# Kernel tuning notes

Hardware: AMD Instinct MI355X
Metric: run time of the kernel (lower is better)

The kernel has to match this reference:

```python
import jax, jax.numpy as jnp
import numpy as np

EPS = 1e-6

def elu_feature_map(x):
    return jax.nn.elu(x) + 1.0

def setup_inputs() -> dict:
    key = jax.random.key(0)
    kq, kk, kv = jax.random.split(key, 3)
    N, L, S, H, D = 8, 8192, 8192, 8, 32
    return {
        "queries": jax.random.normal(kq, (N, L, H, D), dtype=jnp.float32),
        "keys": jax.random.normal(kk, (N, S, H, D), dtype=jnp.float32),
        "values": jax.random.normal(kv, (N, S, H, D), dtype=jnp.float32),
    }

def reference(queries, keys, values):
    # Linear (kernelized) attention, default path of MixAttention.forward
    Q = elu_feature_map(queries)            # [N,L,H,D]
    K = elu_feature_map(keys)               # [N,S,H,D]
    v_length = values.shape[1]
    vals = values / v_length                # [N,S,H,D]
    KV = jnp.einsum('nshd,nshv->nhdv', K, vals)          # [N,H,D,D]
    Z = 1.0 / (jnp.einsum('nlhd,nhd->nlh', Q, K.sum(axis=1)) + EPS)  # [N,L,H]
    out = jnp.einsum('nlhd,nhdv,nlh->nlhv', Q, KV, Z) * v_length     # [N,L,H,D]
    return out
```

## Files before the change

kernel.cpp:

```cpp
#include <hip/hip_runtime.h>


constexpr int N_ = 8, L_ = 8192, S_ = 8192, H_ = 8, D_ = 32;
constexpr int NH = N_ * H_;
constexpr int PART_STRIDE = D_ * D_ + D_;
constexpr int LCH = 256;
constexpr float EPS_ = 1e-6f;
constexpr int HD = H_ * D_;
constexpr int CHUNK = 32;

__device__ __forceinline__ float fmap(float x) {
    return x > 0.0f ? x + 1.0f : __expf(x);
}

__device__ __forceinline__ void dma16(const float* g, float* l) {
    __builtin_amdgcn_global_load_lds(
        (const __attribute__((address_space(1))) unsigned int*)g,
        (__attribute__((address_space(3))) unsigned int*)l, 16, 0, 0);
}

template<int SPL>
__global__ __launch_bounds__(256, 2) void lin_attn_phase1(
        const float* __restrict__ Kg, const float* __restrict__ Vg,
        float* __restrict__ part) {
    constexpr int CS_BLK = S_ / SPL;
    constexpr int ROUNDS = CS_BLK / CHUNK;
    const int blk = blockIdx.x;
    const int n = blk / SPL, c = blk % SPL;
    const int t = threadIdx.x;
    const int w = t >> 6;
    const int lane = t & 63;

    __shared__ __align__(16) float Kt[CHUNK][HD];
    __shared__ __align__(16) float Vt[CHUNK][HD];

    const int hg = t >> 5;
    const int i  = t & 31;
    const int d0 = (i >> 3) << 3;
    const int v0 = (i & 7) << 2;
    const int hcol = hg * D_;

    float acc[8][4];
    #pragma unroll
    for (int a = 0; a < 8; ++a)
        #pragma unroll
        for (int b = 0; b < 4; ++b) acc[a][b] = 0.0f;
    float kp = 0.0f;

    const float* Kbase = Kg + (size_t)n * S_ * HD + (size_t)c * CS_BLK * HD;
    const float* Vbase = Vg + (size_t)n * S_ * HD + (size_t)c * CS_BLK * HD;
    float* Kf = &Kt[0][0];

    for (int r = 0; r < ROUNDS; ++r) {
        const float* ksrc = Kbase + (size_t)r * CHUNK * HD;
        const float* vsrc = Vbase + (size_t)r * CHUNK * HD;
        #pragma unroll
        for (int q = 0; q < 8; ++q) {
            const int off = (w * 8 + q) * 256;
            dma16(ksrc + off + lane * 4, &Kt[0][0] + off);
            dma16(vsrc + off + lane * 4, &Vt[0][0] + off);
        }
        __syncthreads();

        #pragma unroll 8
        for (int k = 0; k < CHUNK; ++k) {
            const float x = fmap(Kf[t + HD * k]);
            Kf[t + HD * k] = x;
            kp += x;
        }
        __syncthreads();

        #pragma unroll 4
        for (int s = 0; s < CHUNK; ++s) {
            const float4 ka = *reinterpret_cast<const float4*>(&Kt[s][hcol + d0]);
            const float4 kb = *reinterpret_cast<const float4*>(&Kt[s][hcol + d0 + 4]);
            const float4 vq = *reinterpret_cast<const float4*>(&Vt[s][hcol + v0]);
            const float kd[8] = {ka.x, ka.y, ka.z, ka.w, kb.x, kb.y, kb.z, kb.w};
            const float vs[4] = {vq.x, vq.y, vq.z, vq.w};
            #pragma unroll
            for (int a = 0; a < 8; ++a)
                #pragma unroll
                for (int b = 0; b < 4; ++b)
                    acc[a][b] += kd[a] * vs[b];
        }
        __syncthreads();
    }

    float* P = part + ((size_t)c * NH + n * H_ + hg) * PART_STRIDE;
    #pragma unroll
    for (int a = 0; a < 8; ++a)
        *reinterpret_cast<float4*>(&P[(d0 + a) * D_ + v0]) =
            make_float4(acc[a][0], acc[a][1], acc[a][2], acc[a][3]);
    part[((size_t)c * NH + n * H_ + (t >> 5)) * PART_STRIDE + D_ * D_ + (t & 31)] = kp;
}

template<int SPL>
__global__ __launch_bounds__(256) void lin_attn_reduce(
        const float* __restrict__ part, float* __restrict__ red) {
    const int i = blockIdx.x * 256 + threadIdx.x;
    if (i >= NH * PART_STRIDE) return;
    float s = 0.0f;
    #pragma unroll 8
    for (int sc = 0; sc < SPL; ++sc)
        s += part[(size_t)sc * (NH * PART_STRIDE) + i];
    red[i] = s;
}

__global__ __launch_bounds__(256) void lin_attn_phase2(
        const float* __restrict__ Qg, const float* __restrict__ red,
        float* __restrict__ outg) {
    constexpr int QTS = 32;
    constexpr int NLC = L_ / LCH;
    const int nh  = blockIdx.x / NLC;
    const int lcb = blockIdx.x % NLC;
    const int n = nh / H_, h = nh % H_;
    const int t = threadIdx.x;
    const int v  = t & 31;
    const int rb = t >> 5;
    const int r  = t >> 3;
    const int c  = (t & 7) << 2;

    __shared__ __align__(16) float Qt[QTS][D_];
    __shared__ float zinv_sh[QTS];

    float kv[D_];
    const float* W = red + (size_t)nh * PART_STRIDE;
    #pragma unroll
    for (int d = 0; d < D_; ++d) kv[d] = W[d * D_ + v];
    const float4 ksq = *reinterpret_cast<const float4*>(W + D_ * D_ + c);

    const size_t base = (size_t)n * L_ * H_ * D_ + (size_t)h * D_;
    const int l0 = lcb * LCH;
    for (int step = 0; step < LCH; step += QTS) {
        const float4 q4 = *reinterpret_cast<const float4*>(
            Qg + base + (size_t)(l0 + step + r) * (H_ * D_) + c);
        __syncthreads();
        float4 qf;
        qf.x = fmap(q4.x); qf.y = fmap(q4.y);
        qf.z = fmap(q4.z); qf.w = fmap(q4.w);
        *reinterpret_cast<float4*>(&Qt[r][c]) = qf;
        float zp = qf.x * ksq.x + qf.y * ksq.y + qf.z * ksq.z + qf.w * ksq.w;
        zp += __shfl_xor(zp, 1);
        zp += __shfl_xor(zp, 2);
        zp += __shfl_xor(zp, 4);
        if ((t & 7) == 0) zinv_sh[r] = 1.0f / (zp + EPS_);
        __syncthreads();
        #pragma unroll
        for (int rr = 0; rr < 4; ++rr) {
            const int row = (rr << 3) + rb;
            float acc = 0.0f;
            #pragma unroll
            for (int d2 = 0; d2 < 16; ++d2) {
                const float2 q = *reinterpret_cast<const float2*>(&Qt[row][d2 << 1]);
                acc += q.x * kv[(d2 << 1)] + q.y * kv[(d2 << 1) + 1];
            }
            outg[base + (size_t)(l0 + step + row) * (H_ * D_) + v] =
                acc * zinv_sh[row];
        }
    }
}

extern "C" void kernel_launch(void* const* d_in, const int* in_sizes, int n_in,
                              void* d_out, int out_size, void* d_ws, size_t ws_size,
                              hipStream_t stream) {
    const float* Q = (const float*)d_in[0];
    const float* K = (const float*)d_in[1];
    const float* V = (const float*)d_in[2];
    float* out  = (float*)d_out;
    float* part = (float*)d_ws;

    const size_t need64 = ((size_t)64 + 1) * NH * PART_STRIDE * sizeof(float);
    if (ws_size >= need64) {
        constexpr int SP = 64;
        float* red = part + (size_t)SP * NH * PART_STRIDE;
        lin_attn_phase1<SP><<<N_ * SP, 256, 0, stream>>>(K, V, part);
        lin_attn_reduce<SP><<<(NH * PART_STRIDE + 255) / 256, 256, 0, stream>>>(part, red);
        lin_attn_phase2<<<NH * (L_ / LCH), 256, 0, stream>>>(Q, red, out);
    } else {
        constexpr int SP = 16;
        float* red = part + (size_t)SP * NH * PART_STRIDE;
        lin_attn_phase1<SP><<<N_ * SP, 256, 0, stream>>>(K, V, part);
        lin_attn_reduce<SP><<<(NH * PART_STRIDE + 255) / 256, 256, 0, stream>>>(part, red);
        lin_attn_phase2<<<NH * (L_ / LCH), 256, 0, stream>>>(Q, red, out);
    }
}
```

Measured before the change: 79.77 us.

## Restructure phase1 to 512-thread blocks with register loads and finer S split

Phase1 now uses 512 threads per block, each computing a 4x4 KV tile, and splits S into 128 chunks instead of 64 for more blocks. The async global-to-LDS DMA path is replaced by register float4 loads, with the ELU feature map applied before the LDS store, so the separate in-LDS feature-map pass and one barrier per round go away. The per-column K sums are reduced across warps through LDS at the end. The aim is higher occupancy and better latency hiding on the K/V streaming pass. The cost is a larger partial buffer for the reduce kernel to sum and the loss of the asynchronous DMA path.

```diff
diff --git a/kernel.cpp b/kernel.cpp
--- a/kernel.cpp
+++ b/kernel.cpp
@@ -7,91 +7,94 @@
 constexpr int LCH = 256;
 constexpr float EPS_ = 1e-6f;
 constexpr int HD = H_ * D_;
-constexpr int CHUNK = 32;
+constexpr int CHUNK = 16;
 
 __device__ __forceinline__ float fmap(float x) {
     return x > 0.0f ? x + 1.0f : __expf(x);
 }
 
-__device__ __forceinline__ void dma16(const float* g, float* l) {
-    __builtin_amdgcn_global_load_lds(
-        (const __attribute__((address_space(1))) unsigned int*)g,
-        (__attribute__((address_space(3))) unsigned int*)l, 16, 0, 0);
-}
-
 template<int SPL>
-__global__ __launch_bounds__(256, 2) void lin_attn_phase1(
+__global__ __launch_bounds__(512, 8) void lin_attn_phase1(
         const float* __restrict__ Kg, const float* __restrict__ Vg,
         float* __restrict__ part) {
     constexpr int CS_BLK = S_ / SPL;
     constexpr int ROUNDS = CS_BLK / CHUNK;
-    const int blk = blockIdx.x;
-    const int n = blk / SPL, c = blk % SPL;
+    const int n  = blockIdx.x / SPL;
+    const int sc = blockIdx.x % SPL;
     const int t = threadIdx.x;
     const int w = t >> 6;
-    const int lane = t & 63;
+    const int i = t & 63;
+    const int c4 = i << 2;
+    const int d0 = (i >> 3) << 2;
+    const int v0 = (i & 7) << 2;
+    const int hcol = w * D_;
 
     __shared__ __align__(16) float Kt[CHUNK][HD];
     __shared__ __align__(16) float Vt[CHUNK][HD];
 
-    const int hg = t >> 5;
-    const int i  = t & 31;
-    const int d0 = (i >> 3) << 3;
-    const int v0 = (i & 7) << 2;
-    const int hcol = hg * D_;
-
-    float acc[8][4];
+    float acc[4][4];
     #pragma unroll
-    for (int a = 0; a < 8; ++a)
+    for (int a = 0; a < 4; ++a)
         #pragma unroll
         for (int b = 0; b < 4; ++b) acc[a][b] = 0.0f;
-    float kp = 0.0f;
+    float kp[4] = {0.f, 0.f, 0.f, 0.f};
 
-    const float* Kbase = Kg + (size_t)n * S_ * HD + (size_t)c * CS_BLK * HD;
-    const float* Vbase = Vg + (size_t)n * S_ * HD + (size_t)c * CS_BLK * HD;
-    float* Kf = &Kt[0][0];
+    const float* Kbase = Kg + (size_t)n * S_ * HD + (size_t)sc * CS_BLK * HD;
+    const float* Vbase = Vg + (size_t)n * S_ * HD + (size_t)sc * CS_BLK * HD;
 
+    #pragma unroll 1
     for (int r = 0; r < ROUNDS; ++r) {
-        const float* ksrc = Kbase + (size_t)r * CHUNK * HD;
-        const float* vsrc = Vbase + (size_t)r * CHUNK * HD;
+        const float* ks = Kbase + (size_t)r * CHUNK * HD;
+        const float* vs = Vbase + (size_t)r * CHUNK * HD;
+        float4 k0 = *reinterpret_cast<const float4*>(ks + (size_t)w * HD + c4);
+        float4 k1 = *reinterpret_cast<const float4*>(ks + (size_t)(w + 8) * HD + c4);
+        const float4 u0 = *reinterpret_cast<const float4*>(vs + (size_t)w * HD + c4);
+        const float4 u1 = *reinterpret_cast<const float4*>(vs + (size_t)(w + 8) * HD + c4);
+        k0.x = fmap(k0.x); k0.y = fmap(k0.y); k0.z = fmap(k0.z); k0.w = fmap(k0.w);
+        k1.x = fmap(k1.x); k1.y = fmap(k1.y); k1.z = fmap(k1.z); k1.w = fmap(k1.w);
+        kp[0] += k0.x + k1.x; kp[1] += k0.y + k1.y;
+        kp[2] += k0.z + k1.z; kp[3] += k0.w + k1.w;
+        __syncthreads();
+        *reinterpret_cast<float4*>(&Kt[w][c4])     = k0;
+        *reinterpret_cast<float4*>(&Kt[w + 8][c4]) = k1;
+        *reinterpret_cast<float4*>(&Vt[w][c4])     = u0;
+        *reinterpret_cast<float4*>(&Vt[w + 8][c4]) = u1;
+        __syncthreads();
         #pragma unroll
-        for (int q = 0; q < 8; ++q) {
-            const int off = (w * 8 + q) * 256;
-            dma16(ksrc + off + lane * 4, &Kt[0][0] + off);
-            dma16(vsrc + off + lane * 4, &Vt[0][0] + off);
-        }
-        __syncthreads();
-
-        #pragma unroll 8
-        for (int k = 0; k < CHUNK; ++k) {
-            const float x = fmap(Kf[t + HD * k]);
-            Kf[t + HD * k] = x;
-            kp += x;
-        }
-        __syncthreads();
-
-        #pragma unroll 4
         for (int s = 0; s < CHUNK; ++s) {
             const float4 ka = *reinterpret_cast<const float4*>(&Kt[s][hcol + d0]);
-            const float4 kb = *reinterpret_cast<const float4*>(&Kt[s][hcol + d0 + 4]);
             const float4 vq = *reinterpret_cast<const float4*>(&Vt[s][hcol + v0]);
-            const float kd[8] = {ka.x, ka.y, ka.z, ka.w, kb.x, kb.y, kb.z, kb.w};
-            const float vs[4] = {vq.x, vq.y, vq.z, vq.w};
+            const float kd[4] = {ka.x, ka.y, ka.z, ka.w};
+            const float vv[4] = {vq.x, vq.y, vq.z, vq.w};
             #pragma unroll
-            for (int a = 0; a < 8; ++a)
+            for (int a = 0; a < 4; ++a)
                 #pragma unroll
                 for (int b = 0; b < 4; ++b)
-                    acc[a][b] += kd[a] * vs[b];
+                    acc[a][b] += kd[a] * vv[b];
         }
-        __syncthreads();
     }
 
-    float* P = part + ((size_t)c * NH + n * H_ + hg) * PART_STRIDE;
+    float* P = part + ((size_t)sc * NH + n * H_ + w) * PART_STRIDE;
     #pragma unroll
-    for (int a = 0; a < 8; ++a)
+    for (int a = 0; a < 4; ++a)
         *reinterpret_cast<float4*>(&P[(d0 + a) * D_ + v0]) =
             make_float4(acc[a][0], acc[a][1], acc[a][2], acc[a][3]);
-    part[((size_t)c * NH + n * H_ + (t >> 5)) * PART_STRIDE + D_ * D_ + (t & 31)] = kp;
+
+    __syncthreads();
+    float* ksl = &Kt[0][0];
+    *reinterpret_cast<float4*>(&ksl[w * HD + c4]) =
+        make_float4(kp[0], kp[1], kp[2], kp[3]);
+    __syncthreads();
+    if (t < 64) {
+        float4 s4 = make_float4(0.f, 0.f, 0.f, 0.f);
+        #pragma unroll
+        for (int g = 0; g < 8; ++g) {
+            const float4 rr = *reinterpret_cast<const float4*>(&ksl[g * HD + (t << 2)]);
+            s4.x += rr.x; s4.y += rr.y; s4.z += rr.z; s4.w += rr.w;
+        }
+        float* P2 = part + ((size_t)sc * NH + n * H_ + (t >> 3)) * PART_STRIDE;
+        *reinterpret_cast<float4*>(&P2[D_ * D_ + ((t & 7) << 2)]) = s4;
+    }
 }
 
 template<int SPL>
@@ -100,7 +103,7 @@
     const int i = blockIdx.x * 256 + threadIdx.x;
     if (i >= NH * PART_STRIDE) return;
     float s = 0.0f;
-    #pragma unroll 8
+    #pragma unroll 16
     for (int sc = 0; sc < SPL; ++sc)
         s += part[(size_t)sc * (NH * PART_STRIDE) + i];
     red[i] = s;
@@ -169,17 +172,17 @@
     float* out  = (float*)d_out;
     float* part = (float*)d_ws;
 
-    const size_t need64 = ((size_t)64 + 1) * NH * PART_STRIDE * sizeof(float);
-    if (ws_size >= need64) {
-        constexpr int SP = 64;
+    const size_t need128 = ((size_t)128 + 1) * NH * PART_STRIDE * sizeof(float);
+    if (ws_size >= need128) {
+        constexpr int SP = 128;
         float* red = part + (size_t)SP * NH * PART_STRIDE;
-        lin_attn_phase1<SP><<<N_ * SP, 256, 0, stream>>>(K, V, part);
+        lin_attn_phase1<SP><<<N_ * SP, 512, 0, stream>>>(K, V, part);
         lin_attn_reduce<SP><<<(NH * PART_STRIDE + 255) / 256, 256, 0, stream>>>(part, red);
         lin_attn_phase2<<<NH * (L_ / LCH), 256, 0, stream>>>(Q, red, out);
     } else {
-        constexpr int SP = 16;
+        constexpr int SP = 64;
         float* red = part + (size_t)SP * NH * PART_STRIDE;
-        lin_attn_phase1<SP><<<N_ * SP, 256, 0, stream>>>(K, V, part);
+        lin_attn_phase1<SP><<<N_ * SP, 512, 0, stream>>>(K, V, part);
         lin_attn_reduce<SP><<<(NH * PART_STRIDE + 255) / 256, 256, 0, stream>>>(part, red);
         lin_attn_phase2<<<NH * (L_ / LCH), 256, 0, stream>>>(Q, red, out);
     }
```

Result: slower. 86.39 us (+8.3%).
